# Kernel tuning notes

Hardware: AMD Instinct MI355X
Metric: run time of the kernel (lower is better)

The kernel has to match this reference:

```python
import jax, jax.numpy as jnp
import numpy as np

N = 100000
E = 3200000
F_IN, H1, H2, C = 256, 64, 32, 1000


def setup_inputs() -> dict:
    key = jax.random.key(0)
    ks = jax.random.split(key, 10)
    x = jax.random.normal(ks[0], (N, F_IN), dtype=jnp.float32)
    edge_src = jax.random.randint(ks[1], (E,), 0, N, dtype=jnp.int32)
    edge_dst = jax.random.randint(ks[2], (E,), 0, N, dtype=jnp.int32)
    s1 = 1.0 / np.sqrt(F_IN)
    s2 = 1.0 / np.sqrt(H1)
    s3 = 1.0 / np.sqrt(H2)
    W1 = jax.random.uniform(ks[3], (F_IN, H1), jnp.float32, -s1, s1)
    b1 = jnp.zeros((H1,), jnp.float32)
    W2 = jax.random.uniform(ks[4], (H1, H2), jnp.float32, -s2, s2)
    b2 = jnp.zeros((H2,), jnp.float32)
    Wfc = jax.random.uniform(ks[5], (H2, C), jnp.float32, -s3, s3)
    bfc = jax.random.uniform(ks[6], (C,), jnp.float32, -s3, s3)
    return {"x": x, "edge_src": edge_src, "edge_dst": edge_dst,
            "W1": W1, "b1": b1, "W2": W2, "b2": b2, "Wfc": Wfc, "bfc": bfc}


def _gcn_conv(x, W, b, src, dst, dinv):
    # PyG GCNConv: linear transform, then normalized scatter-add (with self-loops).
    xw = x @ W  # [N, out]
    coef = dinv[src] * dinv[dst]  # [E]
    msg = xw[src] * coef[:, None]  # gathered, scaled messages
    agg = jax.ops.segment_sum(msg, dst, num_segments=x.shape[0])
    agg = agg + xw * (dinv * dinv)[:, None]  # self-loop contribution
    return agg + b


def reference(x, edge_src, edge_dst, W1, b1, W2, b2, Wfc, bfc):
    n = x.shape[0]
    # degree with self-loops, counted on target nodes
    deg = 1.0 + jax.ops.segment_sum(jnp.ones_like(edge_dst, dtype=x.dtype), edge_dst, num_segments=n)
    dinv = jax.lax.rsqrt(deg)
    h = jax.nn.relu(_gcn_conv(x, W1, b1, edge_src, edge_dst, dinv))
    h = jax.nn.relu(_gcn_conv(h, W2, b2, edge_src, edge_dst, dinv))
    g = jnp.mean(h, axis=0)  # [H2]
    return g @ Wfc + bfc  # [C]
```

## Files before the change

kernel.cpp:

```cpp
#include <hip/hip_runtime.h>

#define N_NODES 100000
#define N_EDGES 3200000
#define F_IN 256
#define H1 64
#define H2 32
#define C_OUT 1000

#define OFF_G      0
#define OFF_DINV   64
#define OFF_CNT    100096
#define OFF_HEAD   200192
#define OFF_OFS    300288
#define OFF_CSR    400384
#define OFF_NODE2  3600384
#define OFF_Y1Q    10000384
#define OFF_Y2Q    11600384

__device__ __forceinline__ unsigned char f2fp8(float x) {
    x = fminf(fmaxf(x, -448.0f), 448.0f);
    unsigned u = __float_as_uint(x);
    unsigned s = (u >> 24) & 0x80u;
    unsigned absu = u & 0x7fffffffu;
    float ax = __uint_as_float(absu);
    if (ax < 0.015625f) {
        int q = __float2int_rn(ax * 512.0f);
        return (unsigned char)(s | (unsigned)q);
    }
    int e = (int)(absu >> 23) - 127;
    unsigned man = absu & 0x7fffffu;
    unsigned m3 = man >> 20;
    unsigned rem = man & 0xFFFFFu;
    if (rem > 0x80000u || (rem == 0x80000u && (m3 & 1u))) m3++;
    if (m3 == 8u) { m3 = 0u; e++; }
    if (e > 8) return (unsigned char)(s | 0x7Eu);
    return (unsigned char)(s | ((unsigned)(e + 7) << 3) | m3);
}

__device__ __forceinline__ float fp8lut_val(int t) {
    int ex = (t >> 3) & 15, man = t & 7;
    int base = ex ? (8 + man) : man;
    float v = ldexpf((float)base, (ex ? ex : 1) - 10);
    return (t & 0x80) ? -v : v;
}

__global__ void k_init(int* __restrict__ head, float* __restrict__ g) {
    int i = blockIdx.x * 256 + threadIdx.x;
    if (i < N_NODES) head[i] = -1;
    if (blockIdx.x == 0 && threadIdx.x < H2) g[threadIdx.x] = 0.0f;
}

__global__ void k_build(const int* __restrict__ src, const int* __restrict__ dst,
                        int* __restrict__ head, int2* __restrict__ node2) {
    int e = blockIdx.x * 256 + threadIdx.x;
    if (e < N_EDGES) {
        int d = dst[e];
        int s = src[e];
        int prev = atomicExch(&head[d], e);
        node2[e] = make_int2(s, prev);
    }
}

__global__ void k_deg(const int* __restrict__ head, const int2* __restrict__ node2,
                      int* __restrict__ cnt, float* __restrict__ dinv) {
    int n = blockIdx.x * 256 + threadIdx.x;
    if (n < N_NODES) {
        int k = 0;
        int e = head[n];
        while (e >= 0) { k++; e = node2[e].y; }
        cnt[n] = k;
        dinv[n] = rsqrtf(1.0f + (float)k);
    }
}

__global__ __launch_bounds__(1024) void k_scan(const int* __restrict__ cnt,
                                               int* __restrict__ ofs) {
    __shared__ int lds[1024];
    const int t = threadIdx.x;
    const int CH = (N_NODES + 1023) / 1024;
    int base = t * CH;
    int end = base + CH; if (end > N_NODES) end = N_NODES;
    int s = 0;
    for (int i = base; i < end; i++) s += cnt[i];
    lds[t] = s;
    __syncthreads();
    for (int off = 1; off < 1024; off <<= 1) {
        int v = (t >= off) ? lds[t - off] : 0;
        __syncthreads();
        lds[t] += v;
        __syncthreads();
    }
    int run = lds[t] - s;
    for (int i = base; i < end; i++) {
        ofs[i] = run;
        run += cnt[i];
    }
    if (t == 1023) ofs[N_NODES] = lds[1023];
}

__global__ __launch_bounds__(256) void k_gemm1(const float* __restrict__ x,
                                               const float* __restrict__ W1,
                                               const float* __restrict__ dinv,
                                               unsigned char* __restrict__ y1q) {
    __shared__ float w[F_IN][H1];
    {
        const float4* Wv = (const float4*)W1;
        float4* wv = (float4*)&w[0][0];
        for (int i = threadIdx.x; i < F_IN * H1 / 4; i += 256) wv[i] = Wv[i];
    }
    __syncthreads();
    int n0 = blockIdx.x * 512 + threadIdx.x;
    int n1 = n0 + 256;
    bool v0 = n0 < N_NODES, v1 = n1 < N_NODES;
    int n0c = v0 ? n0 : 0, n1c = v1 ? n1 : 0;

    float acc0[H1], acc1[H1];
#pragma unroll
    for (int j = 0; j < H1; j++) { acc0[j] = 0.0f; acc1[j] = 0.0f; }

    const float4* xr0 = (const float4*)(x + (size_t)n0c * F_IN);
    const float4* xr1 = (const float4*)(x + (size_t)n1c * F_IN);
#pragma unroll 2
    for (int k0 = 0; k0 < F_IN / 4; k0++) {
        float4 xa = xr0[k0];
        float4 xb = xr1[k0];
#pragma unroll
        for (int d = 0; d < 4; d++) {
            float xv0 = (d == 0 ? xa.x : d == 1 ? xa.y : d == 2 ? xa.z : xa.w);
            float xv1 = (d == 0 ? xb.x : d == 1 ? xb.y : d == 2 ? xb.z : xb.w);
            const float4* wr = (const float4*)&w[k0 * 4 + d][0];
#pragma unroll
            for (int j4 = 0; j4 < H1 / 4; j4++) {
                float4 wq = wr[j4];
                acc0[j4 * 4 + 0] += xv0 * wq.x;
                acc0[j4 * 4 + 1] += xv0 * wq.y;
                acc0[j4 * 4 + 2] += xv0 * wq.z;
                acc0[j4 * 4 + 3] += xv0 * wq.w;
                acc1[j4 * 4 + 0] += xv1 * wq.x;
                acc1[j4 * 4 + 1] += xv1 * wq.y;
                acc1[j4 * 4 + 2] += xv1 * wq.z;
                acc1[j4 * 4 + 3] += xv1 * wq.w;
            }
        }
    }
    if (v0) {
        float dv = dinv[n0];
        unsigned pk[H1 / 4];
#pragma unroll
        for (int q = 0; q < H1 / 4; q++) {
            unsigned b0 = f2fp8(acc0[4 * q + 0] * dv);
            unsigned b1 = f2fp8(acc0[4 * q + 1] * dv);
            unsigned b2 = f2fp8(acc0[4 * q + 2] * dv);
            unsigned b3 = f2fp8(acc0[4 * q + 3] * dv);
            pk[q] = b0 | (b1 << 8) | (b2 << 16) | (b3 << 24);
        }
        uint4* o = (uint4*)(y1q + (size_t)n0 * H1);
#pragma unroll
        for (int q = 0; q < H1 / 16; q++)
            o[q] = make_uint4(pk[q * 4], pk[q * 4 + 1], pk[q * 4 + 2], pk[q * 4 + 3]);
    }
    if (v1) {
        float dv = dinv[n1];
        unsigned pk[H1 / 4];
#pragma unroll
        for (int q = 0; q < H1 / 4; q++) {
            unsigned b0 = f2fp8(acc1[4 * q + 0] * dv);
            unsigned b1 = f2fp8(acc1[4 * q + 1] * dv);
            unsigned b2 = f2fp8(acc1[4 * q + 2] * dv);
            unsigned b3 = f2fp8(acc1[4 * q + 3] * dv);
            pk[q] = b0 | (b1 << 8) | (b2 << 16) | (b3 << 24);
        }
        uint4* o = (uint4*)(y1q + (size_t)n1 * H1);
#pragma unroll
        for (int q = 0; q < H1 / 16; q++)
            o[q] = make_uint4(pk[q * 4], pk[q * 4 + 1], pk[q * 4 + 2], pk[q * 4 + 3]);
    }
}

__global__ __launch_bounds__(256) void k_agg1_gemm2(const unsigned char* __restrict__ y1q,
                                                    const int* __restrict__ head,
                                                    const int2* __restrict__ node2,
                                                    const int* __restrict__ ofs,
                                                    int* __restrict__ csr,
                                                    const float* __restrict__ dinv,
                                                    const float* __restrict__ b1,
                                                    const float* __restrict__ W2,
                                                    unsigned char* __restrict__ y2q) {
    __shared__ float w2s[H1][H2];
    __shared__ float hbuf[8][H1];
    __shared__ float lut[256];
    const int t = threadIdx.x;
    lut[t] = fp8lut_val(t);
    {
        const float4* Wv = (const float4*)W2;
        float4* wv = (float4*)&w2s[0][0];
        for (int i = t; i < H1 * H2 / 4; i += 256) wv[i] = Wv[i];
    }
    __syncthreads();

    const int wid = t >> 6;
    const int lane = t & 63;
    const int c = lane;
    const int n0 = blockIdx.x * 8 + wid * 2;
    const int n1 = n0 + 1;

    float a0 = lut[y1q[(size_t)n0 * H1 + c]];
    float a1 = lut[y1q[(size_t)n1 * H1 + c]];
    int e0 = head[n0], e1 = head[n1];
    const int ofs0 = ofs[n0], ofs1 = ofs[n1];
    int k = 0;
    while (e0 >= 0 && e1 >= 0) {
        int2 v0 = node2[e0];
        int2 v1 = node2[e1];
        if (lane == 0) csr[ofs0 + k] = v0.x;
        if (lane == 1) csr[ofs1 + k] = v1.x;
        a0 += lut[y1q[(size_t)v0.x * H1 + c]];
        a1 += lut[y1q[(size_t)v1.x * H1 + c]];
        e0 = v0.y; e1 = v1.y; k++;
    }
    int k0 = k, k1 = k;
    while (e0 >= 0) {
        int2 v0 = node2[e0];
        if (lane == 0) csr[ofs0 + k0] = v0.x;
        a0 += lut[y1q[(size_t)v0.x * H1 + c]];
        e0 = v0.y; k0++;
    }
    while (e1 >= 0) {
        int2 v1 = node2[e1];
        if (lane == 1) csr[ofs1 + k1] = v1.x;
        a1 += lut[y1q[(size_t)v1.x * H1 + c]];
        e1 = v1.y; k1++;
    }
    float h0 = dinv[n0] * a0 + b1[c];
    float h1v = dinv[n1] * a1 + b1[c];
    hbuf[wid * 2 + 0][c] = h0 > 0.0f ? h0 : 0.0f;
    hbuf[wid * 2 + 1][c] = h1v > 0.0f ? h1v : 0.0f;
    __syncthreads();

    {
        int w = t >> 5, j = t & 31;
        int n2 = blockIdx.x * 8 + w;
        float dot = 0.0f;
#pragma unroll
        for (int cc = 0; cc < H1; cc++) dot += hbuf[w][cc] * w2s[cc][j];
        y2q[(size_t)n2 * H2 + j] = f2fp8(dinv[n2] * dot);
    }
}

__global__ __launch_bounds__(256) void k_agg2_pool(const unsigned char* __restrict__ y2q,
                                                   const int* __restrict__ ofs,
                                                   const int* __restrict__ csr,
                                                   const float* __restrict__ dinv,
                                                   const float* __restrict__ b2,
                                                   float* __restrict__ g) {
    __shared__ float lut[256];
    __shared__ float red[256];
    const int t = threadIdx.x;
    lut[t] = fp8lut_val(t);
    __syncthreads();

    const int n = blockIdx.x * 8 + (t >> 5);
    const int c = t & 31;

    float a = lut[y2q[(size_t)n * H2 + c]];
    const int p0 = ofs[n], p1 = ofs[n + 1];
    for (int p = p0; p < p1; p++) {
        int s = csr[p];
        a += lut[y2q[(size_t)s * H2 + c]];
    }
    float hv = dinv[n] * a + b2[c];
    red[t] = hv > 0.0f ? hv : 0.0f;
    __syncthreads();
    if (t < 128) red[t] += red[t + 128];
    __syncthreads();
    if (t < 64) red[t] += red[t + 64];
    __syncthreads();
    if (t < 32) {
        float s = red[t] + red[t + 32];
        atomicAdd(&g[t], s);
    }
}

__global__ void k_fc(const float* __restrict__ g, const float* __restrict__ Wfc,
                     const float* __restrict__ bfc, float* __restrict__ out) {
    int c = blockIdx.x * 256 + threadIdx.x;
    if (c < C_OUT) {
        const float invn = 1.0f / (float)N_NODES;
        float s = bfc[c];
#pragma unroll
        for (int k = 0; k < H2; k++) s += (g[k] * invn) * Wfc[k * C_OUT + c];
        out[c] = s;
    }
}

extern "C" void kernel_launch(void* const* d_in, const int* in_sizes, int n_in,
                              void* d_out, int out_size, void* d_ws, size_t ws_size,
                              hipStream_t stream) {
    const float* x   = (const float*)d_in[0];
    const int* esrc  = (const int*)d_in[1];
    const int* edst  = (const int*)d_in[2];
    const float* W1  = (const float*)d_in[3];
    const float* b1  = (const float*)d_in[4];
    const float* W2  = (const float*)d_in[5];
    const float* b2  = (const float*)d_in[6];
    const float* Wfc = (const float*)d_in[7];
    const float* bfc = (const float*)d_in[8];
    float* out = (float*)d_out;

    float* ws = (float*)d_ws;
    float* g    = ws + OFF_G;
    float* dinv = ws + OFF_DINV;
    int*   cnt  = (int*)(ws + OFF_CNT);
    int*   head = (int*)(ws + OFF_HEAD);
    int*   ofs  = (int*)(ws + OFF_OFS);
    int*   csr  = (int*)(ws + OFF_CSR);
    int2*  node2 = (int2*)(ws + OFF_NODE2);
    unsigned char* y1q = (unsigned char*)(ws + OFF_Y1Q);
    unsigned char* y2q = (unsigned char*)(ws + OFF_Y2Q);

    const int nb_n = (N_NODES + 255) / 256;
    const int nb_e = (N_EDGES + 255) / 256;

    k_init<<<nb_n, 256, 0, stream>>>(head, g);
    k_build<<<nb_e, 256, 0, stream>>>(esrc, edst, head, node2);
    k_deg<<<nb_n, 256, 0, stream>>>(head, node2, cnt, dinv);
    k_scan<<<1, 1024, 0, stream>>>(cnt, ofs);

    k_gemm1<<<(N_NODES + 511) / 512, 256, 0, stream>>>(x, W1, dinv, y1q);
    k_agg1_gemm2<<<N_NODES / 8, 256, 0, stream>>>(y1q, head, node2, ofs, csr, dinv, b1, W2, y2q);
    k_agg2_pool<<<N_NODES / 8, 256, 0, stream>>>(y2q, ofs, csr, dinv, b2, g);

    k_fc<<<(C_OUT + 255) / 256, 256, 0, stream>>>(g, Wfc, bfc, out);
}
```

Measured before the change: 1.056 ms.

## Fuse degree counting into first GEMM and decode fp8 arithmetically instead of LUT

Merges the linked-list degree walk into the first GEMM kernel, so dinv is computed in registers and one launch plus a dinv reload go away. The walk overlaps with the W1 shared-memory fill, but it now runs in only 196 blocks instead of 391, which reduces the parallelism available to hide the pointer-chasing latency. Separately, the shared-memory fp8 lookup table is replaced with bit-manipulation decoding, which removes LUT setup and a barrier in the aggregation kernels at the cost of a few extra ALU ops per gathered element.

After: 1.029 ms. 1.03x faster.

```diff
diff --git a/kernel.cpp b/kernel.cpp
--- a/kernel.cpp
+++ b/kernel.cpp
@@ -37,11 +37,12 @@
     return (unsigned char)(s | ((unsigned)(e + 7) << 3) | m3);
 }
 
-__device__ __forceinline__ float fp8lut_val(int t) {
-    int ex = (t >> 3) & 15, man = t & 7;
-    int base = ex ? (8 + man) : man;
-    float v = ldexpf((float)base, (ex ? ex : 1) - 10);
-    return (t & 0x80) ? -v : v;
+__device__ __forceinline__ float fp8dec(unsigned b) {
+    unsigned ex = (b >> 3) & 15u, man = b & 7u;
+    float vn = __uint_as_float(((ex + 120u) << 23) | (man << 20));
+    float vs = (float)man * 0.001953125f;
+    float v = ex ? vn : vs;
+    return (b & 0x80u) ? -v : v;
 }
 
 __global__ void k_init(int* __restrict__ head, float* __restrict__ g) {
@@ -58,18 +59,6 @@
         int s = src[e];
         int prev = atomicExch(&head[d], e);
         node2[e] = make_int2(s, prev);
-    }
-}
-
-__global__ void k_deg(const int* __restrict__ head, const int2* __restrict__ node2,
-                      int* __restrict__ cnt, float* __restrict__ dinv) {
-    int n = blockIdx.x * 256 + threadIdx.x;
-    if (n < N_NODES) {
-        int k = 0;
-        int e = head[n];
-        while (e >= 0) { k++; e = node2[e].y; }
-        cnt[n] = k;
-        dinv[n] = rsqrtf(1.0f + (float)k);
     }
 }
 
@@ -98,22 +87,42 @@
     if (t == 1023) ofs[N_NODES] = lds[1023];
 }
 
-__global__ __launch_bounds__(256) void k_gemm1(const float* __restrict__ x,
-                                               const float* __restrict__ W1,
-                                               const float* __restrict__ dinv,
-                                               unsigned char* __restrict__ y1q) {
+__global__ __launch_bounds__(256) void k_gemm1_deg(const float* __restrict__ x,
+                                                   const float* __restrict__ W1,
+                                                   const int* __restrict__ head,
+                                                   const int2* __restrict__ node2,
+                                                   int* __restrict__ cnt,
+                                                   float* __restrict__ dinv,
+                                                   unsigned char* __restrict__ y1q) {
     __shared__ float w[F_IN][H1];
     {
         const float4* Wv = (const float4*)W1;
         float4* wv = (float4*)&w[0][0];
         for (int i = threadIdx.x; i < F_IN * H1 / 4; i += 256) wv[i] = Wv[i];
     }
-    __syncthreads();
+
     int n0 = blockIdx.x * 512 + threadIdx.x;
     int n1 = n0 + 256;
     bool v0 = n0 < N_NODES, v1 = n1 < N_NODES;
     int n0c = v0 ? n0 : 0, n1c = v1 ? n1 : 0;
 
+    int e0 = v0 ? head[n0] : -1;
+    int e1 = v1 ? head[n1] : -1;
+    int k0 = 0, k1 = 0;
+    while (e0 >= 0 && e1 >= 0) {
+        int t0 = node2[e0].y, t1 = node2[e1].y;
+        k0++; k1++;
+        e0 = t0; e1 = t1;
+    }
+    while (e0 >= 0) { k0++; e0 = node2[e0].y; }
+    while (e1 >= 0) { k1++; e1 = node2[e1].y; }
+    float dv0 = rsqrtf(1.0f + (float)k0);
+    float dv1 = rsqrtf(1.0f + (float)k1);
+    if (v0) { cnt[n0] = k0; dinv[n0] = dv0; }
+    if (v1) { cnt[n1] = k1; dinv[n1] = dv1; }
+
+    __syncthreads();
+
     float acc0[H1], acc1[H1];
 #pragma unroll
     for (int j = 0; j < H1; j++) { acc0[j] = 0.0f; acc1[j] = 0.0f; }
@@ -121,14 +130,14 @@
     const float4* xr0 = (const float4*)(x + (size_t)n0c * F_IN);
     const float4* xr1 = (const float4*)(x + (size_t)n1c * F_IN);
 #pragma unroll 2
-    for (int k0 = 0; k0 < F_IN / 4; k0++) {
-        float4 xa = xr0[k0];
-        float4 xb = xr1[k0];
+    for (int kk = 0; kk < F_IN / 4; kk++) {
+        float4 xa = xr0[kk];
+        float4 xb = xr1[kk];
 #pragma unroll
         for (int d = 0; d < 4; d++) {
             float xv0 = (d == 0 ? xa.x : d == 1 ? xa.y : d == 2 ? xa.z : xa.w);
             float xv1 = (d == 0 ? xb.x : d == 1 ? xb.y : d == 2 ? xb.z : xb.w);
-            const float4* wr = (const float4*)&w[k0 * 4 + d][0];
+            const float4* wr = (const float4*)&w[kk * 4 + d][0];
 #pragma unroll
             for (int j4 = 0; j4 < H1 / 4; j4++) {
                 float4 wq = wr[j4];
@@ -144,14 +153,13 @@
         }
     }
     if (v0) {
-        float dv = dinv[n0];
         unsigned pk[H1 / 4];
 #pragma unroll
         for (int q = 0; q < H1 / 4; q++) {
-            unsigned b0 = f2fp8(acc0[4 * q + 0] * dv);
-            unsigned b1 = f2fp8(acc0[4 * q + 1] * dv);
-            unsigned b2 = f2fp8(acc0[4 * q + 2] * dv);
-            unsigned b3 = f2fp8(acc0[4 * q + 3] * dv);
+            unsigned b0 = f2fp8(acc0[4 * q + 0] * dv0);
+            unsigned b1 = f2fp8(acc0[4 * q + 1] * dv0);
+            unsigned b2 = f2fp8(acc0[4 * q + 2] * dv0);
+            unsigned b3 = f2fp8(acc0[4 * q + 3] * dv0);
             pk[q] = b0 | (b1 << 8) | (b2 << 16) | (b3 << 24);
         }
         uint4* o = (uint4*)(y1q + (size_t)n0 * H1);
@@ -160,14 +168,13 @@
             o[q] = make_uint4(pk[q * 4], pk[q * 4 + 1], pk[q * 4 + 2], pk[q * 4 + 3]);
     }
     if (v1) {
-        float dv = dinv[n1];
         unsigned pk[H1 / 4];
 #pragma unroll
         for (int q = 0; q < H1 / 4; q++) {
-            unsigned b0 = f2fp8(acc1[4 * q + 0] * dv);
-            unsigned b1 = f2fp8(acc1[4 * q + 1] * dv);
-            unsigned b2 = f2fp8(acc1[4 * q + 2] * dv);
-            unsigned b3 = f2fp8(acc1[4 * q + 3] * dv);
+            unsigned b0 = f2fp8(acc1[4 * q + 0] * dv1);
+            unsigned b1 = f2fp8(acc1[4 * q + 1] * dv1);
+            unsigned b2 = f2fp8(acc1[4 * q + 2] * dv1);
+            unsigned b3 = f2fp8(acc1[4 * q + 3] * dv1);
             pk[q] = b0 | (b1 << 8) | (b2 << 16) | (b3 << 24);
         }
         uint4* o = (uint4*)(y1q + (size_t)n1 * H1);
@@ -188,9 +195,7 @@
                                                     unsigned char* __restrict__ y2q) {
     __shared__ float w2s[H1][H2];
     __shared__ float hbuf[8][H1];
-    __shared__ float lut[256];
     const int t = threadIdx.x;
-    lut[t] = fp8lut_val(t);
     {
         const float4* Wv = (const float4*)W2;
         float4* wv = (float4*)&w2s[0][0];
@@ -204,8 +209,8 @@
     const int n0 = blockIdx.x * 8 + wid * 2;
     const int n1 = n0 + 1;
 
-    float a0 = lut[y1q[(size_t)n0 * H1 + c]];
-    float a1 = lut[y1q[(size_t)n1 * H1 + c]];
+    float a0 = fp8dec(y1q[(size_t)n0 * H1 + c]);
+    float a1 = fp8dec(y1q[(size_t)n1 * H1 + c]);
     int e0 = head[n0], e1 = head[n1];
     const int ofs0 = ofs[n0], ofs1 = ofs[n1];
     int k = 0;
@@ -214,21 +219,21 @@
         int2 v1 = node2[e1];
         if (lane == 0) csr[ofs0 + k] = v0.x;
         if (lane == 1) csr[ofs1 + k] = v1.x;
-        a0 += lut[y1q[(size_t)v0.x * H1 + c]];
-        a1 += lut[y1q[(size_t)v1.x * H1 + c]];
+        a0 += fp8dec(y1q[(size_t)v0.x * H1 + c]);
+        a1 += fp8dec(y1q[(size_t)v1.x * H1 + c]);
         e0 = v0.y; e1 = v1.y; k++;
     }
     int k0 = k, k1 = k;
     while (e0 >= 0) {
         int2 v0 = node2[e0];
         if (lane == 0) csr[ofs0 + k0] = v0.x;
-        a0 += lut[y1q[(size_t)v0.x * H1 + c]];
+        a0 += fp8dec(y1q[(size_t)v0.x * H1 + c]);
         e0 = v0.y; k0++;
     }
     while (e1 >= 0) {
         int2 v1 = node2[e1];
         if (lane == 1) csr[ofs1 + k1] = v1.x;
-        a1 += lut[y1q[(size_t)v1.x * H1 + c]];
+        a1 += fp8dec(y1q[(size_t)v1.x * H1 + c]);
         e1 = v1.y; k1++;
     }
     float h0 = dinv[n0] * a0 + b1[c];
@@ -253,20 +258,16 @@
                                                    const float* __restrict__ dinv,
                                                    const float* __restrict__ b2,
                                                    float* __restrict__ g) {
-    __shared__ float lut[256];
     __shared__ float red[256];
     const int t = threadIdx.x;
-    lut[t] = fp8lut_val(t);
-    __syncthreads();
-
     const int n = blockIdx.x * 8 + (t >> 5);
     const int c = t & 31;
 
-    float a = lut[y2q[(size_t)n * H2 + c]];
+    float a = fp8dec(y2q[(size_t)n * H2 + c]);
     const int p0 = ofs[n], p1 = ofs[n + 1];
     for (int p = p0; p < p1; p++) {
         int s = csr[p];
-        a += lut[y2q[(size_t)s * H2 + c]];
+        a += fp8dec(y2q[(size_t)s * H2 + c]);
     }
     float hv = dinv[n] * a + b2[c];
     red[t] = hv > 0.0f ? hv : 0.0f;
@@ -323,10 +324,10 @@
 
     k_init<<<nb_n, 256, 0, stream>>>(head, g);
     k_build<<<nb_e, 256, 0, stream>>>(esrc, edst, head, node2);
-    k_deg<<<nb_n, 256, 0, stream>>>(head, node2, cnt, dinv);
+
+    k_gemm1_deg<<<(N_NODES + 511) / 512, 256, 0, stream>>>(x, W1, head, node2, cnt, dinv, y1q);
     k_scan<<<1, 1024, 0, stream>>>(cnt, ofs);
 
-    k_gemm1<<<(N_NODES + 511) / 512, 256, 0, stream>>>(x, W1, dinv, y1q);
     k_agg1_gemm2<<<N_NODES / 8, 256, 0, stream>>>(y1q, head, node2, ofs, csr, dinv, b1, W2, y2q);
     k_agg2_pool<<<N_NODES / 8, 256, 0, stream>>>(y2q, ofs, csr, dinv, b2, g);
 
```
